# Performance work log

Measured on AMD Instinct MI355X. Metric: run time of the kernel, lower is better.

## Reference

```python
import jax, jax.numpy as jnp
import numpy as np

B, S, DIN, DOUT = 4, 2048, 4096, 4096

def setup_inputs() -> dict:
    key = jax.random.key(0)
    k1, k2, k3 = jax.random.split(key, 3)
    x = jax.random.normal(k1, (B, S, DIN), dtype=jnp.float32)
    # symmetric int8 quantized weights, [out_features, in_features]
    int_weight = jax.random.randint(k2, (DOUT, DIN), -128, 128, dtype=jnp.int32).astype(jnp.int8)
    w_scale = jnp.float32(0.01)  # per-tensor scale, zero-point = 0
    fp_bias = jax.random.normal(k3, (DOUT,), dtype=jnp.float32) * 0.01
    return {"x": x, "int_weight": int_weight, "w_scale": w_scale, "fp_bias": fp_bias}

def reference(x, int_weight, w_scale, fp_bias):
    # Dequantize weight: fp32 = int8 * scale (elementwise), then F.linear: x @ w.T + b
    w = int_weight.astype(jnp.float32) * w_scale  # [DOUT, DIN]
    out = jnp.einsum('bsi,oi->bso', x, w) + fp_bias
    return out
```

## Files before the change

kernel.cpp:

```cpp
#include <hip/hip_runtime.h>
#include <hip/hip_bf16.h>

typedef __attribute__((ext_vector_type(8))) short bf16x8;
typedef __attribute__((ext_vector_type(4))) float f32x4;
typedef __attribute__((ext_vector_type(4))) int i32x4;
typedef __attribute__((ext_vector_type(2))) unsigned int u32x2;
typedef __attribute__((ext_vector_type(4))) unsigned int u32x4;

__device__ __forceinline__ unsigned int f2bf(float f) {
    union { float f; unsigned int u; } v; v.f = f;
    unsigned int u = v.u;
    u += 0x7FFFu + ((u >> 16) & 1u);
    return u >> 16;
}

__device__ __forceinline__ void gl_lds16(const void* gptr, void* lptr) {
    __builtin_amdgcn_global_load_lds(
        (const __attribute__((address_space(1))) unsigned int*)gptr,
        (__attribute__((address_space(3))) unsigned int*)lptr, 16, 0, 0);
}

__global__ __launch_bounds__(256) void convert_x_kernel(
    const float* __restrict__ x, unsigned short* __restrict__ xb, long long n8)
{
    long long i = (long long)blockIdx.x * blockDim.x + threadIdx.x;
    const long long stride = (long long)gridDim.x * blockDim.x;
    for (; i < n8; i += stride) {
        const f32x4* p = (const f32x4*)(x + i * 8);
        f32x4 v0 = p[0], v1 = p[1];
        u32x4 q;
        q[0] = f2bf(v0[0]) | (f2bf(v0[1]) << 16);
        q[1] = f2bf(v0[2]) | (f2bf(v0[3]) << 16);
        q[2] = f2bf(v1[0]) | (f2bf(v1[1]) << 16);
        q[3] = f2bf(v1[2]) | (f2bf(v1[3]) << 16);
        *(u32x4*)(xb + i * 8) = q;
    }
}

__global__ __launch_bounds__(256) void convert_w_kernel(
    const int* __restrict__ w, unsigned short* __restrict__ wb, long long n8)
{
    long long i = (long long)blockIdx.x * blockDim.x + threadIdx.x;
    const long long stride = (long long)gridDim.x * blockDim.x;
    for (; i < n8; i += stride) {
        const i32x4* p = (const i32x4*)(w + i * 8);
        i32x4 v0 = p[0], v1 = p[1];
        u32x4 q;
        q[0] = f2bf((float)v0[0]) | (f2bf((float)v0[1]) << 16);
        q[1] = f2bf((float)v0[2]) | (f2bf((float)v0[3]) << 16);
        q[2] = f2bf((float)v1[0]) | (f2bf((float)v1[1]) << 16);
        q[3] = f2bf((float)v1[2]) | (f2bf((float)v1[3]) << 16);
        *(u32x4*)(wb + i * 8) = q;
    }
}

__global__ __launch_bounds__(512, 2) void gemm256_kernel(
    const unsigned short* __restrict__ A, const unsigned short* __restrict__ Bw,
    const float* __restrict__ wscale, const float* __restrict__ bias,
    float* __restrict__ out, int M, int N, int K)
{
    __shared__ unsigned char lds[163840];
    const int B0OFF = 98304;

    const int tid  = threadIdx.x;
    const int lane = tid & 63;
    const int wid  = tid >> 6;
    const int wr   = wid >> 1;
    const int wc   = wid & 1;

    const int ntn = N >> 8;
    const int nwg = gridDim.x;
    int bid = blockIdx.x;
    if ((nwg & 7) == 0) {
        const int cpx = nwg >> 3;
        bid = (bid & 7) * cpx + (bid >> 3);
    }
    const int bm = bid / ntn;
    const int bn = bid % ntn;
    const int NT = K >> 6;

    const char* Abase = (const char*)(A  + (size_t)bm * 256 * K);
    const char* Bbase = (const char*)(Bw + (size_t)bn * 256 * K);
    const size_t rowb = (size_t)K * 2;

    const int s_colb = (((lane & 7) ^ (lane >> 3)) << 4);
    const int s_rsub = wid * 8 + (lane >> 3);
    const int s_ldso = wid * 1024 + lane * 16;

    auto stageHalf = [&](const char* gRowBase, char* lhalf) {
#pragma unroll
        for (int q = 0; q < 2; ++q)
            gl_lds16(gRowBase + (size_t)(q * 64 + s_rsub) * rowb + s_colb,
                     lhalf + q * 8192 + s_ldso);
    };
    auto Ag = [&](int kt, int h) { return Abase + (size_t)kt * 128 + (size_t)(h * 128) * rowb; };
    auto Bg = [&](int kt, int h) { return Bbase + (size_t)kt * 128 + (size_t)(h * 128) * rowb; };

    const int arow = (wr * 64  + (lane & 15)) * 128;
    const int brow = (wc * 128 + (lane & 15)) * 128;
    const int csw0 = (((lane >> 4) * 16))      ^ ((lane & 7) << 4);
    const int csw1 = (((lane >> 4) * 16) + 64) ^ ((lane & 7) << 4);

    f32x4 acc[4][8];
#pragma unroll
    for (int mi = 0; mi < 4; ++mi)
#pragma unroll
        for (int ni = 0; ni < 8; ++ni)
            acc[mi][ni] = (f32x4){0.f, 0.f, 0.f, 0.f};

    bf16x8 a0[4], a1[4], bA[4], bB[4];

    stageHalf(Ag(0, 0), (char*)lds + 0);
    stageHalf(Ag(0, 1), (char*)lds + 16384);
    stageHalf(Bg(0, 0), (char*)lds + B0OFF);
    stageHalf(Bg(0, 1), (char*)lds + B0OFF + 16384);
    if (NT > 1) {
        stageHalf(Ag(1, 0), (char*)lds + 32768);
        stageHalf(Ag(1, 1), (char*)lds + 32768 + 16384);
        asm volatile("s_waitcnt vmcnt(4)" ::: "memory");
    } else {
        asm volatile("s_waitcnt vmcnt(0)" ::: "memory");
    }
    __builtin_amdgcn_sched_barrier(0);
    asm volatile("s_barrier" ::: "memory");
    {
        const char* Al = (const char*)lds;
        const char* Bl = (const char*)lds + B0OFF;
#pragma unroll
        for (int fm = 0; fm < 4; ++fm) a0[fm] = *(const bf16x8*)(Al + arow + fm * 2048 + csw0);
#pragma unroll
        for (int fn = 0; fn < 4; ++fn) bA[fn] = *(const bf16x8*)(Bl + brow + fn * 2048 + csw0);
    }

    int acur = 0, anxt = 32768, ann = 65536;
    int bcur = B0OFF, both = B0OFF + 32768;

    for (int kt = 0; kt < NT; ++kt) {
        const char* Al = (const char*)lds + acur;
        const char* Bl = (const char*)lds + bcur;
        char* Bs  = (char*)lds + both;
        char* As2 = (char*)lds + ann;

        if (kt + 1 < NT) stageHalf(Bg(kt + 1, 0), Bs);
#pragma unroll
        for (int fm = 0; fm < 4; ++fm) a1[fm] = *(const bf16x8*)(Al + arow + fm * 2048 + csw1);
#pragma unroll
        for (int fn = 0; fn < 4; ++fn) bB[fn] = *(const bf16x8*)(Bl + brow + (fn + 4) * 2048 + csw0);
        __builtin_amdgcn_s_setprio(1);
#pragma unroll
        for (int fm = 0; fm < 4; ++fm)
#pragma unroll
            for (int fn = 0; fn < 4; ++fn)
                acc[fm][fn] = __builtin_amdgcn_mfma_f32_16x16x32_bf16(a0[fm], bA[fn], acc[fm][fn], 0, 0, 0);
        __builtin_amdgcn_s_setprio(0);

        if (kt + 1 < NT) stageHalf(Bg(kt + 1, 1), Bs + 16384);
#pragma unroll
        for (int fn = 0; fn < 4; ++fn) bA[fn] = *(const bf16x8*)(Bl + brow + fn * 2048 + csw1);
        __builtin_amdgcn_s_setprio(1);
#pragma unroll
        for (int fm = 0; fm < 4; ++fm)
#pragma unroll
            for (int fn = 0; fn < 4; ++fn)
                acc[fm][fn + 4] = __builtin_amdgcn_mfma_f32_16x16x32_bf16(a0[fm], bB[fn], acc[fm][fn + 4], 0, 0, 0);
        __builtin_amdgcn_s_setprio(0);

        if (kt + 2 < NT) stageHalf(Ag(kt + 2, 0), As2);
#pragma unroll
        for (int fn = 0; fn < 4; ++fn) bB[fn] = *(const bf16x8*)(Bl + brow + (fn + 4) * 2048 + csw1);
        __builtin_amdgcn_s_setprio(1);
#pragma unroll
        for (int fm = 0; fm < 4; ++fm)
#pragma unroll
            for (int fn = 0; fn < 4; ++fn)
                acc[fm][fn] = __builtin_amdgcn_mfma_f32_16x16x32_bf16(a1[fm], bA[fn], acc[fm][fn], 0, 0, 0);
        __builtin_amdgcn_s_setprio(0);

        if (kt + 2 < NT) stageHalf(Ag(kt + 2, 1), As2 + 16384);
        if (kt + 1 < NT) {
            if (kt + 2 < NT) { asm volatile("s_waitcnt vmcnt(4)" ::: "memory"); }
            else             { asm volatile("s_waitcnt vmcnt(0)" ::: "memory"); }
            __builtin_amdgcn_sched_barrier(0);
            asm volatile("s_barrier" ::: "memory");
            const char* nAl = (const char*)lds + anxt;
            const char* nBl = (const char*)lds + both;
#pragma unroll
            for (int fm = 0; fm < 4; ++fm) a0[fm] = *(const bf16x8*)(nAl + arow + fm * 2048 + csw0);
#pragma unroll
            for (int fn = 0; fn < 4; ++fn) bA[fn] = *(const bf16x8*)(nBl + brow + fn * 2048 + csw0);
        }
        __builtin_amdgcn_s_setprio(1);
#pragma unroll
        for (int fm = 0; fm < 4; ++fm)
#pragma unroll
            for (int fn = 0; fn < 4; ++fn)
                acc[fm][fn + 4] = __builtin_amdgcn_mfma_f32_16x16x32_bf16(a1[fm], bB[fn], acc[fm][fn + 4], 0, 0, 0);
        __builtin_amdgcn_s_setprio(0);
        asm volatile("s_barrier" ::: "memory");

        const int at = acur; acur = anxt; anxt = ann; ann = at;
        const int bt = bcur; bcur = both; both = bt;
    }

    const float scale = *wscale;
    const int orow0 = bm * 256 + wr * 64  + ((lane >> 4) << 2);
    const int ocol0 = bn * 256 + wc * 128 + (lane & 15);
#pragma unroll
    for (int fn = 0; fn < 8; ++fn) {
        const int col = ocol0 + 16 * fn;
        const float bb = bias[col];
#pragma unroll
        for (int fm = 0; fm < 4; ++fm) {
            const int row0 = orow0 + 16 * fm;
#pragma unroll
            for (int i = 0; i < 4; ++i)
                out[(size_t)(row0 + i) * N + col] = acc[fm][fn][i] * scale + bb;
        }
    }
}

__device__ __forceinline__ int swz(int row, int byte_in_row) {
    return row * 128 + (byte_in_row ^ ((row & 7) << 4));
}

__global__ __launch_bounds__(256) void qlinear_fused_kernel(
    const float* __restrict__ X, const int* __restrict__ W,
    const float* __restrict__ wscale, const float* __restrict__ bias,
    float* __restrict__ out, int M, int N, int K)
{
    __shared__ unsigned char smem[32768];

    const int t    = threadIdx.x;
    const int lane = t & 63;
    const int wid  = t >> 6;
    const int wr   = wid >> 1;
    const int wc   = wid & 1;

    const int ntn = N >> 7;
    const int bm  = blockIdx.x / ntn;
    const int bn  = blockIdx.x % ntn;
    const int NT  = K >> 6;

    const float* Ab = X + (size_t)bm * 128 * K;
    const int*   Bb = W + (size_t)bn * 128 * K;

    const int srow = t >> 4, sc4 = t & 15;

    f32x4 av[8];
    i32x4 bv[8];

    auto loadAB = [&](int kt) {
        const float* Ap = Ab + kt * 64 + sc4 * 4;
#pragma unroll
        for (int l = 0; l < 8; ++l)
            av[l] = *(const f32x4*)(Ap + (size_t)(srow + 16 * l) * K);
        const int* Bp = Bb + kt * 64 + sc4 * 4;
#pragma unroll
        for (int l = 0; l < 8; ++l)
            bv[l] = *(const i32x4*)(Bp + (size_t)(srow + 16 * l) * K);
    };

    auto writeAB = [&]() {
#pragma unroll
        for (int l = 0; l < 8; ++l) {
            const int row = srow + 16 * l;
            u32x2 pk;
            pk[0] = f2bf(av[l][0]) | (f2bf(av[l][1]) << 16);
            pk[1] = f2bf(av[l][2]) | (f2bf(av[l][3]) << 16);
            *(u32x2*)(smem + swz(row, sc4 * 8)) = pk;
        }
#pragma unroll
        for (int l = 0; l < 8; ++l) {
            const int row = srow + 16 * l;
            u32x2 pk;
            pk[0] = f2bf((float)bv[l][0]) | (f2bf((float)bv[l][1]) << 16);
            pk[1] = f2bf((float)bv[l][2]) | (f2bf((float)bv[l][3]) << 16);
            *(u32x2*)(smem + 16384 + swz(row, sc4 * 8)) = pk;
        }
    };

    f32x4 acc[4][4];
#pragma unroll
    for (int mi = 0; mi < 4; ++mi)
#pragma unroll
        for (int ni = 0; ni < 4; ++ni)
            acc[mi][ni] = (f32x4){0.f, 0.f, 0.f, 0.f};

    const int kbyte = (lane >> 4) * 16;
    const int afr   = wr * 64 + (lane & 15);
    const int bfr   = wc * 64 + (lane & 15);

    loadAB(0);

    for (int kt = 0; kt < NT; ++kt) {
        writeAB();
        __syncthreads();
        if (kt + 1 < NT) loadAB(kt + 1);
#pragma unroll
        for (int kk = 0; kk < 2; ++kk) {
            bf16x8 a[4], b[4];
#pragma unroll
            for (int mi = 0; mi < 4; ++mi)
                a[mi] = *(const bf16x8*)(smem + swz(afr + 16 * mi, kk * 64 + kbyte));
#pragma unroll
            for (int ni = 0; ni < 4; ++ni)
                b[ni] = *(const bf16x8*)(smem + 16384 + swz(bfr + 16 * ni, kk * 64 + kbyte));
#pragma unroll
            for (int mi = 0; mi < 4; ++mi)
#pragma unroll
                for (int ni = 0; ni < 4; ++ni)
                    acc[mi][ni] = __builtin_amdgcn_mfma_f32_16x16x32_bf16(
                        a[mi], b[ni], acc[mi][ni], 0, 0, 0);
        }
        __syncthreads();
    }

    const float scale = *wscale;
    const int orow0 = bm * 128 + wr * 64 + ((lane >> 4) << 2);
    const int ocol0 = bn * 128 + wc * 64 + (lane & 15);
#pragma unroll
    for (int ni = 0; ni < 4; ++ni) {
        const int col = ocol0 + 16 * ni;
        const float bb = bias[col];
#pragma unroll
        for (int mi = 0; mi < 4; ++mi) {
            const int row0 = orow0 + 16 * mi;
#pragma unroll
            for (int i = 0; i < 4; ++i)
                out[(size_t)(row0 + i) * N + col] = acc[mi][ni][i] * scale + bb;
        }
    }
}

extern "C" void kernel_launch(void* const* d_in, const int* in_sizes, int n_in,
                              void* d_out, int out_size, void* d_ws, size_t ws_size,
                              hipStream_t stream) {
    const float* x      = (const float*)d_in[0];
    const int*   w      = (const int*)d_in[1];
    const float* wscale = (const float*)d_in[2];
    const float* bias   = (const float*)d_in[3];
    float*       out    = (float*)d_out;

    const int DOUT = in_sizes[3];
    const int DIN  = in_sizes[1] / DOUT;
    const int M    = in_sizes[0] / DIN;

    const size_t xb_bytes = (size_t)M * DIN * 2;
    const size_t wb_bytes = (size_t)DOUT * DIN * 2;

    if (ws_size >= xb_bytes + wb_bytes && (M % 256) == 0 && (DOUT % 256) == 0
        && (DIN % 64) == 0 && (DIN / 64) >= 2) {
        unsigned short* xb = (unsigned short*)d_ws;
        unsigned short* wb = (unsigned short*)((char*)d_ws + xb_bytes);

        const long long nx8 = (long long)M * DIN / 8;
        const long long nw8 = (long long)DOUT * DIN / 8;
        convert_x_kernel<<<2048, 256, 0, stream>>>(x, xb, nx8);
        convert_w_kernel<<<2048, 256, 0, stream>>>(w, wb, nw8);

        dim3 grid((M / 256) * (DOUT / 256));
        gemm256_kernel<<<grid, 512, 0, stream>>>(xb, wb, wscale, bias, out, M, DOUT, DIN);
    } else {
        dim3 grid((M / 128) * (DOUT / 128));
        qlinear_fused_kernel<<<grid, 256, 0, stream>>>(x, w, wscale, bias, out, M, DOUT, DIN);
    }
}
```

Measured before the change: 280.4 us.

## Retile GEMM to 256x128 tiles with 256 threads and K-step of 32

Shrinks the block tile from 256x256 with 512 threads and K-step 64 to 256x128 with 256 threads and K-step 32, with a new LDS swizzle and staging scheme. Each wave now computes a 128x64 subtile. LDS use drops from 160KB to 64KB, aiming to fit more blocks per CU and double the grid size. The trade-off is lower data reuse per tile and more barriers per unit of K.

```diff
diff --git a/kernel.cpp b/kernel.cpp
--- a/kernel.cpp
+++ b/kernel.cpp
@@ -54,13 +54,13 @@
     }
 }
 
-__global__ __launch_bounds__(512, 2) void gemm256_kernel(
+__global__ __launch_bounds__(256, 2) void gemm256_kernel(
     const unsigned short* __restrict__ A, const unsigned short* __restrict__ Bw,
     const float* __restrict__ wscale, const float* __restrict__ bias,
     float* __restrict__ out, int M, int N, int K)
 {
-    __shared__ unsigned char lds[163840];
-    const int B0OFF = 98304;
+    __shared__ unsigned char lds[65536];
+    const int BOFF = 49152;
 
     const int tid  = threadIdx.x;
     const int lane = tid & 63;
@@ -68,7 +68,7 @@
     const int wr   = wid >> 1;
     const int wc   = wid & 1;
 
-    const int ntn = N >> 8;
+    const int ntn = N >> 7;
     const int nwg = gridDim.x;
     int bid = blockIdx.x;
     if ((nwg & 7) == 0) {
@@ -77,46 +77,46 @@
     }
     const int bm = bid / ntn;
     const int bn = bid % ntn;
-    const int NT = K >> 6;
+    const int NT = K >> 5;
 
     const char* Abase = (const char*)(A  + (size_t)bm * 256 * K);
-    const char* Bbase = (const char*)(Bw + (size_t)bn * 256 * K);
+    const char* Bbase = (const char*)(Bw + (size_t)bn * 128 * K);
     const size_t rowb = (size_t)K * 2;
 
-    const int s_colb = (((lane & 7) ^ (lane >> 3)) << 4);
-    const int s_rsub = wid * 8 + (lane >> 3);
-    const int s_ldso = wid * 1024 + lane * 16;
-
-    auto stageHalf = [&](const char* gRowBase, char* lhalf) {
-#pragma unroll
-        for (int q = 0; q < 2; ++q)
-            gl_lds16(gRowBase + (size_t)(q * 64 + s_rsub) * rowb + s_colb,
-                     lhalf + q * 8192 + s_ldso);
+    const int slog = (tid & 7) ^ ((tid >> 3) & 7);
+    const int sR   = 2 * (tid >> 3) + (slog >> 2);
+    const int sC   = (slog & 3) * 16;
+
+    auto stageA = [&](const char* g, char* dst) {
+#pragma unroll
+        for (int p = 0; p < 4; ++p)
+            gl_lds16(g + (size_t)(p * 64 + sR) * rowb + sC, dst + p * 4096 + tid * 16);
     };
-    auto Ag = [&](int kt, int h) { return Abase + (size_t)kt * 128 + (size_t)(h * 128) * rowb; };
-    auto Bg = [&](int kt, int h) { return Bbase + (size_t)kt * 128 + (size_t)(h * 128) * rowb; };
-
-    const int arow = (wr * 64  + (lane & 15)) * 128;
-    const int brow = (wc * 128 + (lane & 15)) * 128;
-    const int csw0 = (((lane >> 4) * 16))      ^ ((lane & 7) << 4);
-    const int csw1 = (((lane >> 4) * 16) + 64) ^ ((lane & 7) << 4);
-
-    f32x4 acc[4][8];
-#pragma unroll
-    for (int mi = 0; mi < 4; ++mi)
-#pragma unroll
-        for (int ni = 0; ni < 8; ++ni)
+    auto stageB = [&](const char* g, char* dst) {
+#pragma unroll
+        for (int p = 0; p < 2; ++p)
+            gl_lds16(g + (size_t)(p * 64 + sR) * rowb + sC, dst + p * 4096 + tid * 16);
+    };
+    auto Ag = [&](int kt) { return Abase + (size_t)kt * 64; };
+    auto Bg = [&](int kt) { return Bbase + (size_t)kt * 64; };
+
+    const int aps   = (((lane & 1) << 2) | (lane >> 4)) ^ ((lane & 15) >> 1);
+    const int aBase = (wr * 64 + ((lane & 15) >> 1)) * 128 + aps * 16;
+    const int bBase = (wc * 32 + ((lane & 15) >> 1)) * 128 + aps * 16;
+
+    f32x4 acc[8][4];
+#pragma unroll
+    for (int mi = 0; mi < 8; ++mi)
+#pragma unroll
+        for (int ni = 0; ni < 4; ++ni)
             acc[mi][ni] = (f32x4){0.f, 0.f, 0.f, 0.f};
 
-    bf16x8 a0[4], a1[4], bA[4], bB[4];
-
-    stageHalf(Ag(0, 0), (char*)lds + 0);
-    stageHalf(Ag(0, 1), (char*)lds + 16384);
-    stageHalf(Bg(0, 0), (char*)lds + B0OFF);
-    stageHalf(Bg(0, 1), (char*)lds + B0OFF + 16384);
+    bf16x8 a[4], a4[4], b[4];
+
+    stageA(Ag(0), (char*)lds + 0);
+    stageB(Bg(0), (char*)lds + BOFF);
     if (NT > 1) {
-        stageHalf(Ag(1, 0), (char*)lds + 32768);
-        stageHalf(Ag(1, 1), (char*)lds + 32768 + 16384);
+        stageA(Ag(1), (char*)lds + 16384);
         asm volatile("s_waitcnt vmcnt(4)" ::: "memory");
     } else {
         asm volatile("s_waitcnt vmcnt(0)" ::: "memory");
@@ -125,77 +125,52 @@
     asm volatile("s_barrier" ::: "memory");
     {
         const char* Al = (const char*)lds;
-        const char* Bl = (const char*)lds + B0OFF;
-#pragma unroll
-        for (int fm = 0; fm < 4; ++fm) a0[fm] = *(const bf16x8*)(Al + arow + fm * 2048 + csw0);
-#pragma unroll
-        for (int fn = 0; fn < 4; ++fn) bA[fn] = *(const bf16x8*)(Bl + brow + fn * 2048 + csw0);
-    }
-
-    int acur = 0, anxt = 32768, ann = 65536;
-    int bcur = B0OFF, both = B0OFF + 32768;
+        const char* Bl = (const char*)lds + BOFF;
+#pragma unroll
+        for (int fm = 0; fm < 4; ++fm) a[fm] = *(const bf16x8*)(Al + aBase + fm * 1024);
+#pragma unroll
+        for (int fn = 0; fn < 4; ++fn) b[fn] = *(const bf16x8*)(Bl + bBase + fn * 1024);
+    }
+
+    int acur = 0, anxt = 16384, ann = 32768;
+    int bcur = BOFF, both = BOFF + 8192;
 
     for (int kt = 0; kt < NT; ++kt) {
         const char* Al = (const char*)lds + acur;
-        const char* Bl = (const char*)lds + bcur;
-        char* Bs  = (char*)lds + both;
-        char* As2 = (char*)lds + ann;
-
-        if (kt + 1 < NT) stageHalf(Bg(kt + 1, 0), Bs);
-#pragma unroll
-        for (int fm = 0; fm < 4; ++fm) a1[fm] = *(const bf16x8*)(Al + arow + fm * 2048 + csw1);
-#pragma unroll
-        for (int fn = 0; fn < 4; ++fn) bB[fn] = *(const bf16x8*)(Bl + brow + (fn + 4) * 2048 + csw0);
+
+        if (kt + 1 < NT) stageB(Bg(kt + 1), (char*)lds + both);
+#pragma unroll
+        for (int fm = 0; fm < 4; ++fm) a4[fm] = *(const bf16x8*)(Al + aBase + (fm + 4) * 1024);
         __builtin_amdgcn_s_setprio(1);
 #pragma unroll
         for (int fm = 0; fm < 4; ++fm)
 #pragma unroll
             for (int fn = 0; fn < 4; ++fn)
-                acc[fm][fn] = __builtin_amdgcn_mfma_f32_16x16x32_bf16(a0[fm], bA[fn], acc[fm][fn], 0, 0, 0);
+                acc[fm][fn] = __builtin_amdgcn_mfma_f32_16x16x32_bf16(a[fm], b[fn], acc[fm][fn], 0, 0, 0);
         __builtin_amdgcn_s_setprio(0);
 
-        if (kt + 1 < NT) stageHalf(Bg(kt + 1, 1), Bs + 16384);
-#pragma unroll
-        for (int fn = 0; fn < 4; ++fn) bA[fn] = *(const bf16x8*)(Bl + brow + fn * 2048 + csw1);
-        __builtin_amdgcn_s_setprio(1);
-#pragma unroll
-        for (int fm = 0; fm < 4; ++fm)
-#pragma unroll
-            for (int fn = 0; fn < 4; ++fn)
-                acc[fm][fn + 4] = __builtin_amdgcn_mfma_f32_16x16x32_bf16(a0[fm], bB[fn], acc[fm][fn + 4], 0, 0, 0);
-        __builtin_amdgcn_s_setprio(0);
-
-        if (kt + 2 < NT) stageHalf(Ag(kt + 2, 0), As2);
-#pragma unroll
-        for (int fn = 0; fn < 4; ++fn) bB[fn] = *(const bf16x8*)(Bl + brow + (fn + 4) * 2048 + csw1);
-        __builtin_amdgcn_s_setprio(1);
-#pragma unroll
-        for (int fm = 0; fm < 4; ++fm)
-#pragma unroll
-            for (int fn = 0; fn < 4; ++fn)
-                acc[fm][fn] = __builtin_amdgcn_mfma_f32_16x16x32_bf16(a1[fm], bA[fn], acc[fm][fn], 0, 0, 0);
-        __builtin_amdgcn_s_setprio(0);
-
-        if (kt + 2 < NT) stageHalf(Ag(kt + 2, 1), As2 + 16384);
+        if (kt + 2 < NT) stageA(Ag(kt + 2), (char*)lds + ann);
         if (kt + 1 < NT) {
             if (kt + 2 < NT) { asm volatile("s_waitcnt vmcnt(4)" ::: "memory"); }
             else             { asm volatile("s_waitcnt vmcnt(0)" ::: "memory"); }
             __builtin_amdgcn_sched_barrier(0);
             asm volatile("s_barrier" ::: "memory");
+        }
+        __builtin_amdgcn_s_setprio(1);
+#pragma unroll
+        for (int fm = 0; fm < 4; ++fm)
+#pragma unroll
+            for (int fn = 0; fn < 4; ++fn)
+                acc[fm + 4][fn] = __builtin_amdgcn_mfma_f32_16x16x32_bf16(a4[fm], b[fn], acc[fm + 4][fn], 0, 0, 0);
+        __builtin_amdgcn_s_setprio(0);
+        if (kt + 1 < NT) {
             const char* nAl = (const char*)lds + anxt;
             const char* nBl = (const char*)lds + both;
 #pragma unroll
-            for (int fm = 0; fm < 4; ++fm) a0[fm] = *(const bf16x8*)(nAl + arow + fm * 2048 + csw0);
-#pragma unroll
-            for (int fn = 0; fn < 4; ++fn) bA[fn] = *(const bf16x8*)(nBl + brow + fn * 2048 + csw0);
-        }
-        __builtin_amdgcn_s_setprio(1);
-#pragma unroll
-        for (int fm = 0; fm < 4; ++fm)
-#pragma unroll
-            for (int fn = 0; fn < 4; ++fn)
-                acc[fm][fn + 4] = __builtin_amdgcn_mfma_f32_16x16x32_bf16(a1[fm], bB[fn], acc[fm][fn + 4], 0, 0, 0);
-        __builtin_amdgcn_s_setprio(0);
+            for (int fm = 0; fm < 4; ++fm) a[fm] = *(const bf16x8*)(nAl + aBase + fm * 1024);
+#pragma unroll
+            for (int fn = 0; fn < 4; ++fn) b[fn] = *(const bf16x8*)(nBl + bBase + fn * 1024);
+        }
         asm volatile("s_barrier" ::: "memory");
 
         const int at = acur; acur = anxt; anxt = ann; ann = at;
@@ -203,14 +178,14 @@
     }
 
     const float scale = *wscale;
-    const int orow0 = bm * 256 + wr * 64  + ((lane >> 4) << 2);
-    const int ocol0 = bn * 256 + wc * 128 + (lane & 15);
-#pragma unroll
-    for (int fn = 0; fn < 8; ++fn) {
+    const int orow0 = bm * 256 + wr * 128 + ((lane >> 4) << 2);
+    const int ocol0 = bn * 128 + wc * 64  + (lane & 15);
+#pragma unroll
+    for (int fn = 0; fn < 4; ++fn) {
         const int col = ocol0 + 16 * fn;
         const float bb = bias[col];
 #pragma unroll
-        for (int fm = 0; fm < 4; ++fm) {
+        for (int fm = 0; fm < 8; ++fm) {
             const int row0 = orow0 + 16 * fm;
 #pragma unroll
             for (int i = 0; i < 4; ++i)
@@ -348,8 +323,8 @@
     const size_t xb_bytes = (size_t)M * DIN * 2;
     const size_t wb_bytes = (size_t)DOUT * DIN * 2;
 
-    if (ws_size >= xb_bytes + wb_bytes && (M % 256) == 0 && (DOUT % 256) == 0
-        && (DIN % 64) == 0 && (DIN / 64) >= 2) {
+    if (ws_size >= xb_bytes + wb_bytes && (M % 256) == 0 && (DOUT % 128) == 0
+        && (DIN % 32) == 0 && (DIN / 32) >= 2) {
         unsigned short* xb = (unsigned short*)d_ws;
         unsigned short* wb = (unsigned short*)((char*)d_ws + xb_bytes);
 
@@ -358,8 +333,8 @@
         convert_x_kernel<<<2048, 256, 0, stream>>>(x, xb, nx8);
         convert_w_kernel<<<2048, 256, 0, stream>>>(w, wb, nw8);
 
-        dim3 grid((M / 256) * (DOUT / 256));
-        gemm256_kernel<<<grid, 512, 0, stream>>>(xb, wb, wscale, bias, out, M, DOUT, DIN);
+        dim3 grid((M / 256) * (DOUT / 128));
+        gemm256_kernel<<<grid, 256, 0, stream>>>(xb, wb, wscale, bias, out, M, DOUT, DIN);
     } else {
         dim3 grid((M / 128) * (DOUT / 128));
         qlinear_fused_kernel<<<grid, 256, 0, stream>>>(x, w, wscale, bias, out, M, DOUT, DIN);
```

New measurement: 328.8 us. +17.3%, slower.

## Remap waves to 2x4 grid with barrier-interleaved LDS reads and MFMA phases

Applied to the files above, without the earlier changes.

Changes the wave layout from 4x2 (64x128 per wave) to 2x4 (128x64 per wave) and restructures the main loop into four phases. Each phase loads its fragments from LDS just before use instead of prefetching them into the previous phase, and s_barriers are placed around every MFMA block so that the waves' LDS reads and compute run in lockstep, ping-pong style. The aim is to lower register pressure by keeping one A/B fragment set instead of two, and to keep LDS traffic from overlapping MFMA execution across waves. The risk is that the extra barriers and the lost prefetch overlap expose LDS latency.

```diff
diff --git a/kernel.cpp b/kernel.cpp
--- a/kernel.cpp
+++ b/kernel.cpp
@@ -65,8 +65,8 @@
     const int tid  = threadIdx.x;
     const int lane = tid & 63;
     const int wid  = tid >> 6;
-    const int wr   = wid >> 1;
-    const int wc   = wid & 1;
+    const int wr   = wid >> 2;
+    const int wc   = wid & 3;
 
     const int ntn = N >> 8;
     const int nwg = gridDim.x;
@@ -96,19 +96,19 @@
     auto Ag = [&](int kt, int h) { return Abase + (size_t)kt * 128 + (size_t)(h * 128) * rowb; };
     auto Bg = [&](int kt, int h) { return Bbase + (size_t)kt * 128 + (size_t)(h * 128) * rowb; };
 
-    const int arow = (wr * 64  + (lane & 15)) * 128;
-    const int brow = (wc * 128 + (lane & 15)) * 128;
+    const int aBase = (wr * 128 + (lane & 15)) * 128;
+    const int bBase = (wc * 64  + (lane & 15)) * 128;
     const int csw0 = (((lane >> 4) * 16))      ^ ((lane & 7) << 4);
     const int csw1 = (((lane >> 4) * 16) + 64) ^ ((lane & 7) << 4);
 
-    f32x4 acc[4][8];
-#pragma unroll
-    for (int mi = 0; mi < 4; ++mi)
-#pragma unroll
-        for (int ni = 0; ni < 8; ++ni)
+    f32x4 acc[8][4];
+#pragma unroll
+    for (int mi = 0; mi < 8; ++mi)
+#pragma unroll
+        for (int ni = 0; ni < 4; ++ni)
             acc[mi][ni] = (f32x4){0.f, 0.f, 0.f, 0.f};
 
-    bf16x8 a0[4], a1[4], bA[4], bB[4];
+    bf16x8 ra[4], rb[4];
 
     stageHalf(Ag(0, 0), (char*)lds + 0);
     stageHalf(Ag(0, 1), (char*)lds + 16384);
@@ -123,14 +123,6 @@
     }
     __builtin_amdgcn_sched_barrier(0);
     asm volatile("s_barrier" ::: "memory");
-    {
-        const char* Al = (const char*)lds;
-        const char* Bl = (const char*)lds + B0OFF;
-#pragma unroll
-        for (int fm = 0; fm < 4; ++fm) a0[fm] = *(const bf16x8*)(Al + arow + fm * 2048 + csw0);
-#pragma unroll
-        for (int fn = 0; fn < 4; ++fn) bA[fn] = *(const bf16x8*)(Bl + brow + fn * 2048 + csw0);
-    }
 
     int acur = 0, anxt = 32768, ann = 65536;
     int bcur = B0OFF, both = B0OFF + 32768;
@@ -141,61 +133,65 @@
         char* Bs  = (char*)lds + both;
         char* As2 = (char*)lds + ann;
 
+#pragma unroll
+        for (int fm = 0; fm < 4; ++fm) ra[fm] = *(const bf16x8*)(Al + aBase + fm * 2048 + csw0);
+#pragma unroll
+        for (int fn = 0; fn < 4; ++fn) rb[fn] = *(const bf16x8*)(Bl + bBase + fn * 2048 + csw0);
         if (kt + 1 < NT) stageHalf(Bg(kt + 1, 0), Bs);
-#pragma unroll
-        for (int fm = 0; fm < 4; ++fm) a1[fm] = *(const bf16x8*)(Al + arow + fm * 2048 + csw1);
-#pragma unroll
-        for (int fn = 0; fn < 4; ++fn) bB[fn] = *(const bf16x8*)(Bl + brow + (fn + 4) * 2048 + csw0);
+        asm volatile("s_barrier" ::: "memory");
         __builtin_amdgcn_s_setprio(1);
 #pragma unroll
         for (int fm = 0; fm < 4; ++fm)
 #pragma unroll
             for (int fn = 0; fn < 4; ++fn)
-                acc[fm][fn] = __builtin_amdgcn_mfma_f32_16x16x32_bf16(a0[fm], bA[fn], acc[fm][fn], 0, 0, 0);
+                acc[fm][fn] = __builtin_amdgcn_mfma_f32_16x16x32_bf16(ra[fm], rb[fn], acc[fm][fn], 0, 0, 0);
         __builtin_amdgcn_s_setprio(0);
-
+        asm volatile("s_barrier" ::: "memory");
+
+#pragma unroll
+        for (int fm = 0; fm < 4; ++fm) ra[fm] = *(const bf16x8*)(Al + aBase + (fm + 4) * 2048 + csw0);
         if (kt + 1 < NT) stageHalf(Bg(kt + 1, 1), Bs + 16384);
-#pragma unroll
-        for (int fn = 0; fn < 4; ++fn) bA[fn] = *(const bf16x8*)(Bl + brow + fn * 2048 + csw1);
+        asm volatile("s_barrier" ::: "memory");
         __builtin_amdgcn_s_setprio(1);
 #pragma unroll
         for (int fm = 0; fm < 4; ++fm)
 #pragma unroll
             for (int fn = 0; fn < 4; ++fn)
-                acc[fm][fn + 4] = __builtin_amdgcn_mfma_f32_16x16x32_bf16(a0[fm], bB[fn], acc[fm][fn + 4], 0, 0, 0);
+                acc[fm + 4][fn] = __builtin_amdgcn_mfma_f32_16x16x32_bf16(ra[fm], rb[fn], acc[fm + 4][fn], 0, 0, 0);
         __builtin_amdgcn_s_setprio(0);
-
+        asm volatile("s_barrier" ::: "memory");
+
+#pragma unroll
+        for (int fm = 0; fm < 4; ++fm) ra[fm] = *(const bf16x8*)(Al + aBase + fm * 2048 + csw1);
+#pragma unroll
+        for (int fn = 0; fn < 4; ++fn) rb[fn] = *(const bf16x8*)(Bl + bBase + fn * 2048 + csw1);
         if (kt + 2 < NT) stageHalf(Ag(kt + 2, 0), As2);
-#pragma unroll
-        for (int fn = 0; fn < 4; ++fn) bB[fn] = *(const bf16x8*)(Bl + brow + (fn + 4) * 2048 + csw1);
+        asm volatile("s_barrier" ::: "memory");
         __builtin_amdgcn_s_setprio(1);
 #pragma unroll
         for (int fm = 0; fm < 4; ++fm)
 #pragma unroll
             for (int fn = 0; fn < 4; ++fn)
-                acc[fm][fn] = __builtin_amdgcn_mfma_f32_16x16x32_bf16(a1[fm], bA[fn], acc[fm][fn], 0, 0, 0);
+                acc[fm][fn] = __builtin_amdgcn_mfma_f32_16x16x32_bf16(ra[fm], rb[fn], acc[fm][fn], 0, 0, 0);
         __builtin_amdgcn_s_setprio(0);
-
+        asm volatile("s_barrier" ::: "memory");
+
+#pragma unroll
+        for (int fm = 0; fm < 4; ++fm) ra[fm] = *(const bf16x8*)(Al + aBase + (fm + 4) * 2048 + csw1);
         if (kt + 2 < NT) stageHalf(Ag(kt + 2, 1), As2 + 16384);
+        asm volatile("s_barrier" ::: "memory");
+        __builtin_amdgcn_s_setprio(1);
+#pragma unroll
+        for (int fm = 0; fm < 4; ++fm)
+#pragma unroll
+            for (int fn = 0; fn < 4; ++fn)
+                acc[fm + 4][fn] = __builtin_amdgcn_mfma_f32_16x16x32_bf16(ra[fm], rb[fn], acc[fm + 4][fn], 0, 0, 0);
+        __builtin_amdgcn_s_setprio(0);
         if (kt + 1 < NT) {
             if (kt + 2 < NT) { asm volatile("s_waitcnt vmcnt(4)" ::: "memory"); }
             else             { asm volatile("s_waitcnt vmcnt(0)" ::: "memory"); }
             __builtin_amdgcn_sched_barrier(0);
-            asm volatile("s_barrier" ::: "memory");
-            const char* nAl = (const char*)lds + anxt;
-            const char* nBl = (const char*)lds + both;
-#pragma unroll
-            for (int fm = 0; fm < 4; ++fm) a0[fm] = *(const bf16x8*)(nAl + arow + fm * 2048 + csw0);
-#pragma unroll
-            for (int fn = 0; fn < 4; ++fn) bA[fn] = *(const bf16x8*)(nBl + brow + fn * 2048 + csw0);
-        }
-        __builtin_amdgcn_s_setprio(1);
-#pragma unroll
-        for (int fm = 0; fm < 4; ++fm)
-#pragma unroll
-            for (int fn = 0; fn < 4; ++fn)
-                acc[fm][fn + 4] = __builtin_amdgcn_mfma_f32_16x16x32_bf16(a1[fm], bB[fn], acc[fm][fn + 4], 0, 0, 0);
-        __builtin_amdgcn_s_setprio(0);
+        }
         asm volatile("s_barrier" ::: "memory");
 
         const int at = acur; acur = anxt; anxt = ann; ann = at;
@@ -203,14 +199,14 @@
     }
 
     const float scale = *wscale;
-    const int orow0 = bm * 256 + wr * 64  + ((lane >> 4) << 2);
-    const int ocol0 = bn * 256 + wc * 128 + (lane & 15);
-#pragma unroll
-    for (int fn = 0; fn < 8; ++fn) {
+    const int orow0 = bm * 256 + wr * 128 + ((lane >> 4) << 2);
+    const int ocol0 = bn * 256 + wc * 64  + (lane & 15);
+#pragma unroll
+    for (int fn = 0; fn < 4; ++fn) {
         const int col = ocol0 + 16 * fn;
         const float bb = bias[col];
 #pragma unroll
-        for (int fm = 0; fm < 4; ++fm) {
+        for (int fm = 0; fm < 8; ++fm) {
             const int row0 = orow0 + 16 * fm;
 #pragma unroll
             for (int i = 0; i < 4; ++i)
```

New measurement: 298.1 us. 6.3% more time.
